# Kernel tuning notes

Measured on AMD Instinct MI355X. Metric: run time of the kernel, lower is better.

## Reference

```python
import jax, jax.numpy as jnp
import numpy as np

B, T, D, HS = 4, 2048, 1024, 64

def setup_inputs() -> dict:
    key = jax.random.key(0)
    kx, kk, kq, kv = jax.random.split(key, 4)
    scale = 1.0 / np.sqrt(D)
    return {
        "x": jax.random.normal(kx, (B, T, D), dtype=jnp.float32),
        "Wk": jax.random.normal(kk, (D, HS), dtype=jnp.float32) * scale,
        "Wq": jax.random.normal(kq, (D, HS), dtype=jnp.float32) * scale,
        "Wv": jax.random.normal(kv, (D, HS), dtype=jnp.float32) * scale,
    }

def reference(x, Wk, Wq, Wv):
    # x: [B, T, D]; projections to [B, T, HS]
    k = jnp.einsum("btd,dh->bth", x, Wk)
    q = jnp.einsum("btd,dh->bth", x, Wq)
    v = jnp.einsum("btd,dh->bth", x, Wv)
    # scores [B, T, T]; NOTE: original multiplies by sqrt(head_size) (faithful)
    att = jnp.einsum("bth,bsh->bts", q, k) * jnp.sqrt(jnp.float32(k.shape[-1]))
    Tq = x.shape[1]
    causal = jnp.tril(jnp.ones((Tq, Tq), dtype=bool))
    att = jnp.where(causal[None, :, :], att, -jnp.inf)
    p = jax.nn.softmax(att, axis=-1)
    # dropout = identity (eval mode)
    return jnp.einsum("bts,bsh->bth", p, v)
```

## Files before the change

kernel.cpp:

```cpp
#include <hip/hip_runtime.h>

#define Bn 4
#define Tn 2048
#define Dn 1024
#define HSn 64

typedef __attribute__((ext_vector_type(8))) short bf16x8;
typedef __attribute__((ext_vector_type(4))) float f32x4;
typedef __attribute__((ext_vector_type(4))) short s16x4;
typedef unsigned short u16;
typedef unsigned int u32;

__device__ __forceinline__ u16 f2bf_rne(float x) {
    u32 u = __float_as_uint(x);
    return (u16)((u + 0x7FFFu + ((u >> 16) & 1u)) >> 16);
}
__device__ __forceinline__ u16 f2bf_trunc(float x) {
    return (u16)(__float_as_uint(x) >> 16);
}
__device__ __forceinline__ float bf2f(u16 h) {
    return __uint_as_float(((u32)h) << 16);
}

#define GLL16(g, l)                                                        \
    __builtin_amdgcn_global_load_lds(                                      \
        (const __attribute__((address_space(1))) void*)(g),                \
        (__attribute__((address_space(3))) void*)(l), 16, 0, 0)

__global__ __launch_bounds__(256) void wprep_kernel(
    const float* __restrict__ Wk, const float* __restrict__ Wq,
    const float* __restrict__ Wv, u16* __restrict__ wtp)
{
    __shared__ float ws_[64][65];
    const int kb = blockIdx.x;
    const int w  = blockIdx.y;
    const float* __restrict__ W = (w == 0) ? Wk : (w == 1) ? Wq : Wv;
    const float scale = (w == 1) ? 8.0f : 1.0f;
    const int t = threadIdx.x;

    {
        const int kl = t >> 2, hq = t & 3;
        #pragma unroll
        for (int i = 0; i < 4; ++i) {
            float4 f = *(const float4*)(W + (size_t)(kb * 64 + kl) * 64 + hq * 16 + i * 4);
            ws_[kl][hq * 16 + i * 4 + 0] = f.x; ws_[kl][hq * 16 + i * 4 + 1] = f.y;
            ws_[kl][hq * 16 + i * 4 + 2] = f.z; ws_[kl][hq * 16 + i * 4 + 3] = f.w;
        }
    }
    __syncthreads();

    const int h = t & 63, quarter = t >> 6;
    const int n = w * 64 + h;
    const int ks = kb * 2 + (quarter >> 1);
    const int k_in0 = (quarter & 1) * 16;
    u16 hib[16], lob[16];
    #pragma unroll
    for (int j = 0; j < 16; ++j) {
        float v = ws_[quarter * 16 + j][h] * scale;
        u16 hi = f2bf_trunc(v);
        hib[j] = hi;
        lob[j] = f2bf_trunc(v - bf2f(hi));
    }
    u16* dst = wtp + (size_t)n * 2048 + ks * 64;
    *(uint4*)(dst + k_in0)          = *(const uint4*)&hib[0];
    *(uint4*)(dst + k_in0 + 8)      = *(const uint4*)&hib[8];
    *(uint4*)(dst + 32 + k_in0)     = *(const uint4*)&lob[0];
    *(uint4*)(dst + 32 + k_in0 + 8) = *(const uint4*)&lob[8];
}

#define NKS 32
#define XB(P) (smem + (P) * 4096)
#define BB(P) (smem + 12288 + (P) * 24576)

__global__ __launch_bounds__(512) void proj_gemm(
    const float* __restrict__ x, const u16* __restrict__ wtp,
    u16* __restrict__ qh8, u16* __restrict__ ql8,
    u16* __restrict__ kth, u16* __restrict__ ktl,
    u16* __restrict__ vtt)
{
    __shared__ __align__(16) unsigned char smem[86016];

    const int tid  = threadIdx.x;
    const int wave = tid >> 6, lane = tid & 63;
    const int lo4  = lane & 15, g = lane >> 4;
    const int row0 = blockIdx.x * 32;
    const int rt   = wave >> 2;
    const int cbase = (wave & 3) * 3;
    const int rl = rt * 16 + lo4;

    f32x4 acc[3];
    #pragma unroll
    for (int c = 0; c < 3; ++c) acc[c] = (f32x4){0.f, 0.f, 0.f, 0.f};

    const int xr = (tid >> 3) & 31, xc = tid & 7;
    const int xsw = (xc ^ (xr & 7)) << 2;
    const float* xsrc0 = x + (size_t)(row0 + xr) * Dn + xsw;

    #define STAGE(P, KS)                                                     \
        {                                                                    \
            if (tid < 256) GLL16(xsrc0 + (KS) * 32, XB(P) + tid * 16);       \
            _Pragma("unroll")                                                \
            for (int i = 0; i < 3; ++i) {                                    \
                const int c = i * 512 + tid;                                 \
                const int n_ = c >> 3, p_ = c & 7;                           \
                const int l_ = p_ ^ (n_ & 7);                                \
                const u16* src = wtp + (size_t)n_ * 2048 + (KS) * 64         \
                                 + ((l_ & 3) << 3) + ((l_ >> 2) << 5);       \
                GLL16(src, BB(P) + c * 16);                                  \
            }                                                                \
        }

    #define COMPUTE(P, KS)                                                   \
        {                                                                    \
            bf16x8 ah, al;                                                   \
            {                                                                \
                const unsigned char* xb = XB(P) + rl * 128;                  \
                f32x4 f0 = *(const f32x4*)(xb + (((2 * g + 0) ^ (rl & 7)) << 4)); \
                f32x4 f1 = *(const f32x4*)(xb + (((2 * g + 1) ^ (rl & 7)) << 4)); \
                _Pragma("unroll")                                            \
                for (int jj = 0; jj < 4; ++jj) {                             \
                    u16 h0 = f2bf_trunc(f0[jj]);                             \
                    ah[jj] = (short)h0;                                      \
                    al[jj] = (short)f2bf_trunc(f0[jj] - bf2f(h0));           \
                    u16 h1 = f2bf_trunc(f1[jj]);                             \
                    ah[4 + jj] = (short)h1;                                  \
                    al[4 + jj] = (short)f2bf_trunc(f1[jj] - bf2f(h1));       \
                }                                                            \
            }                                                                \
            _Pragma("unroll")                                                \
            for (int ct = 0; ct < 3; ++ct) {                                 \
                const int n = (cbase + ct) * 16 + lo4;                       \
                const unsigned char* bb = BB(P) + n * 128;                   \
                bf16x8 bh = *(const bf16x8*)(bb + (((g)     ^ (n & 7)) << 4)); \
                bf16x8 bl = *(const bf16x8*)(bb + (((4 + g) ^ (n & 7)) << 4)); \
                acc[ct] = __builtin_amdgcn_mfma_f32_16x16x32_bf16(ah, bh, acc[ct], 0, 0, 0); \
                acc[ct] = __builtin_amdgcn_mfma_f32_16x16x32_bf16(al, bh, acc[ct], 0, 0, 0); \
                acc[ct] = __builtin_amdgcn_mfma_f32_16x16x32_bf16(ah, bl, acc[ct], 0, 0, 0); \
            }                                                                \
        }

    STAGE(0, 0)
    STAGE(1, 1)
    int pb = 0;
    for (int ks = 0; ks < NKS; ++ks) {
        if (ks == NKS - 1) {
            asm volatile("s_waitcnt vmcnt(0)" ::: "memory");
        } else if (wave < 4) {
            asm volatile("s_waitcnt vmcnt(4)" ::: "memory");
        } else {
            asm volatile("s_waitcnt vmcnt(3)" ::: "memory");
        }
        __builtin_amdgcn_s_barrier();
        asm volatile("" ::: "memory");

        int ps = pb + 2; if (ps >= 3) ps -= 3;
        if (ks + 2 < NKS) STAGE(ps, ks + 2)
        COMPUTE(pb, ks)
        pb = (pb == 2) ? 0 : pb + 1;
    }

    const int grow = row0 + rt * 16 + g * 4;
    const int bb_ = grow >> 11, tl = grow & 2047;
    #pragma unroll
    for (int ct = 0; ct < 3; ++ct) {
        const int n = (cbase + ct) * 16 + lo4;
        if (n < 64) {
            const int ch = n >> 5, gi = (n >> 3) & 3, e = n & 7;
            const size_t base = (size_t)bb_ * 131072
                + (size_t)(((((tl >> 4) * 2 + ch) * 4 + gi) * 16 + (tl & 15)) * 8 + e);
            #pragma unroll
            for (int reg = 0; reg < 4; ++reg) {
                float v = acc[ct][reg];
                u16 hi = f2bf_trunc(v);
                kth[base + reg * 8] = hi;
                ktl[base + reg * 8] = f2bf_trunc(v - bf2f(hi));
            }
        } else if (n < 128) {
            #pragma unroll
            for (int reg = 0; reg < 4; ++reg) {
                float v = acc[ct][reg];
                u16 hi = f2bf_trunc(v);
                qh8[(size_t)(grow + reg) * HSn + (n - 64)] = hi;
                ql8[(size_t)(grow + reg) * HSn + (n - 64)] = f2bf_trunc(v - bf2f(hi));
            }
        } else {
            const int h = n - 128;
            s16x4 pack;
            #pragma unroll
            for (int reg = 0; reg < 4; ++reg)
                pack[reg] = (short)f2bf_rne(acc[ct][reg]);
            const size_t vidx = (size_t)bb_ * 131072
                + (size_t)((tl >> 5) * 2048 + (h >> 4) * 512 + (h & 15) * 32
                           + ((tl >> 3) & 3) * 8 + (tl & 7));
            *(s16x4*)(vtt + vidx) = pack;
        }
    }
}

struct KVset {
    bf16x8 kh0[2], kh1[2], kl0[2], kl1[2], vf[4];
};

__global__ __launch_bounds__(256, 2) void attn_kernel(
    const u16* __restrict__ qh8, const u16* __restrict__ ql8,
    const u16* __restrict__ kth, const u16* __restrict__ ktl,
    const u16* __restrict__ vtt, float* __restrict__ out)
{
    __shared__ __align__(16) unsigned char pbuf[4096];
    __shared__ __align__(16) float om_s[4][16][64];
    __shared__ float ml_s[4][16][2];

    const int tid  = threadIdx.x;
    const int wave = tid >> 6, lane = tid & 63;
    const int lo4  = lane & 15, g = lane >> 4;

    const int sblk = blockIdx.x >> 8, c = blockIdx.x & 255;
    const int tb = sblk ? 127 - (c >> 1) : (c >> 1);
    const int b  = 2 * sblk + (c & 1);
    const int t0 = tb * 16;

    const u16* qhp = qh8 + ((size_t)b * Tn + t0) * HSn;
    const u16* qlp = ql8 + ((size_t)b * Tn + t0) * HSn;
    const u16* kthb = kth + (size_t)b * 131072;
    const u16* ktlb = ktl + (size_t)b * 131072;
    const u16* vttb = vtt + (size_t)b * 131072;
    const int klane = lane * 8;
    const int vlane = lo4 * 32 + g * 8;

    bf16x8 qfh[2], qfl[2];
    #pragma unroll
    for (int ch = 0; ch < 2; ++ch) {
        qfh[ch] = *(const bf16x8*)(qhp + lo4 * HSn + ch * 32 + g * 8);
        qfl[ch] = *(const bf16x8*)(qlp + lo4 * HSn + ch * 32 + g * 8);
    }

    f32x4 O[4];
    #pragma unroll
    for (int n = 0; n < 4; ++n) O[n] = (f32x4){0.f, 0.f, 0.f, 0.f};
    float mrow[4], lrow[4];
    #pragma unroll
    for (int r = 0; r < 4; ++r) { mrow[r] = -1e30f; lrow[r] = 0.f; }

    const int nt = (t0 + 15) / 32 + 1;
    unsigned char* myPB = pbuf + wave * 1024;

    #define LOADSET(S, J)                                                     \
        {                                                                     \
            const u16* kb_ = kthb + (size_t)(2 * (J)) * 1024 + klane;         \
            const u16* lb_ = ktlb + (size_t)(2 * (J)) * 1024 + klane;         \
            S.kh0[0] = *(const bf16x8*)(kb_);                                 \
            S.kh1[0] = *(const bf16x8*)(kb_ + 512);                           \
            S.kh0[1] = *(const bf16x8*)(kb_ + 1024);                          \
            S.kh1[1] = *(const bf16x8*)(kb_ + 1536);                          \
            S.kl0[0] = *(const bf16x8*)(lb_);                                 \
            S.kl1[0] = *(const bf16x8*)(lb_ + 512);                           \
            S.kl0[1] = *(const bf16x8*)(lb_ + 1024);                          \
            S.kl1[1] = *(const bf16x8*)(lb_ + 1536);                          \
            const u16* vb_ = vttb + (size_t)(J) * 2048 + vlane;               \
            S.vf[0] = *(const bf16x8*)(vb_);                                  \
            S.vf[1] = *(const bf16x8*)(vb_ + 512);                            \
            S.vf[2] = *(const bf16x8*)(vb_ + 1024);                           \
            S.vf[3] = *(const bf16x8*)(vb_ + 1536);                           \
        }

    #define COMPUTE_ATT(S, J)                                                 \
        {                                                                     \
            const int s0 = (J) * 32;                                          \
            f32x4 accS[2];                                                    \
            __builtin_amdgcn_s_setprio(1);                                    \
            _Pragma("unroll")                                                 \
            for (int sb = 0; sb < 2; ++sb) {                                  \
                f32x4 a = (f32x4){0.f, 0.f, 0.f, 0.f};                        \
                a = __builtin_amdgcn_mfma_f32_16x16x32_bf16(qfh[0], S.kh0[sb], a, 0, 0, 0); \
                a = __builtin_amdgcn_mfma_f32_16x16x32_bf16(qfh[1], S.kh1[sb], a, 0, 0, 0); \
                a = __builtin_amdgcn_mfma_f32_16x16x32_bf16(qfl[0], S.kh0[sb], a, 0, 0, 0); \
                a = __builtin_amdgcn_mfma_f32_16x16x32_bf16(qfl[1], S.kh1[sb], a, 0, 0, 0); \
                a = __builtin_amdgcn_mfma_f32_16x16x32_bf16(qfh[0], S.kl0[sb], a, 0, 0, 0); \
                a = __builtin_amdgcn_mfma_f32_16x16x32_bf16(qfh[1], S.kl1[sb], a, 0, 0, 0); \
                accS[sb] = a;                                                 \
            }                                                                 \
            __builtin_amdgcn_s_setprio(0);                                    \
            _Pragma("unroll")                                                 \
            for (int reg = 0; reg < 4; ++reg) {                               \
                const int tg  = t0 + g * 4 + reg;                             \
                const int sg0 = s0 + lo4;                                     \
                const int sg1 = s0 + 16 + lo4;                                \
                float v0 = (sg0 <= tg) ? accS[0][reg] : -1e30f;               \
                float v1 = (sg1 <= tg) ? accS[1][reg] : -1e30f;               \
                float mt = fmaxf(v0, v1);                                     \
                mt = fmaxf(mt, __shfl_xor(mt, 1));                            \
                mt = fmaxf(mt, __shfl_xor(mt, 2));                            \
                mt = fmaxf(mt, __shfl_xor(mt, 4));                            \
                mt = fmaxf(mt, __shfl_xor(mt, 8));                            \
                float mn = fmaxf(mrow[reg], mt);                              \
                float p0 = (sg0 <= tg) ? __expf(v0 - mn) : 0.f;               \
                float p1 = (sg1 <= tg) ? __expf(v1 - mn) : 0.f;               \
                float ps = p0 + p1;                                           \
                ps += __shfl_xor(ps, 1);                                      \
                ps += __shfl_xor(ps, 2);                                      \
                ps += __shfl_xor(ps, 4);                                      \
                ps += __shfl_xor(ps, 8);                                      \
                float alpha = __expf(mrow[reg] - mn);                         \
                lrow[reg] = lrow[reg] * alpha + ps;                           \
                mrow[reg] = mn;                                               \
                _Pragma("unroll")                                             \
                for (int n = 0; n < 4; ++n) O[n][reg] *= alpha;               \
                const int irow = g * 4 + reg;                                 \
                *(u16*)(myPB + ((irow * 64 + lo4 * 2) ^ (reg << 4)))      = f2bf_rne(p0); \
                *(u16*)(myPB + ((irow * 64 + 32 + lo4 * 2) ^ (reg << 4))) = f2bf_rne(p1); \
            }                                                                 \
            bf16x8 pf = *(const bf16x8*)(myPB + ((lo4 * 64 + 16 * g) ^ ((lo4 & 3) << 4))); \
            __builtin_amdgcn_s_setprio(1);                                    \
            _Pragma("unroll")                                                 \
            for (int n = 0; n < 4; ++n)                                       \
                O[n] = __builtin_amdgcn_mfma_f32_16x16x32_bf16(pf, S.vf[n], O[n], 0, 0, 0); \
            __builtin_amdgcn_s_setprio(0);                                    \
        }

    KVset A, B;
    int j = wave;
    if (j < nt) LOADSET(A, j)
    while (j < nt) {
        if (j + 4 < nt) LOADSET(B, j + 4)
        COMPUTE_ATT(A, j)
        if (j + 4 < nt) {
            if (j + 8 < nt) LOADSET(A, j + 8)
            COMPUTE_ATT(B, j + 4)
        }
        j += 8;
    }

    #pragma unroll
    for (int n = 0; n < 4; ++n)
        #pragma unroll
        for (int reg = 0; reg < 4; ++reg)
            om_s[wave][g * 4 + reg][n * 16 + lo4] = O[n][reg];
    if (lo4 == 0) {
        #pragma unroll
        for (int reg = 0; reg < 4; ++reg) {
            ml_s[wave][g * 4 + reg][0] = mrow[reg];
            ml_s[wave][g * 4 + reg][1] = lrow[reg];
        }
    }
    __syncthreads();

    const int r  = tid >> 4;
    const int h4 = (tid & 15) * 4;
    float mw[4], lw[4], mstar = -1e30f;
    #pragma unroll
    for (int w = 0; w < 4; ++w) {
        mw[w] = ml_s[w][r][0];
        lw[w] = ml_s[w][r][1];
        mstar = fmaxf(mstar, mw[w]);
    }
    float lstar = 0.f, ew[4];
    #pragma unroll
    for (int w = 0; w < 4; ++w) { ew[w] = __expf(mw[w] - mstar); lstar += lw[w] * ew[w]; }
    float4 a4 = {0.f, 0.f, 0.f, 0.f};
    #pragma unroll
    for (int w = 0; w < 4; ++w) {
        float4 t4 = *(const float4*)&om_s[w][r][h4];
        a4.x += t4.x * ew[w]; a4.y += t4.y * ew[w];
        a4.z += t4.z * ew[w]; a4.w += t4.w * ew[w];
    }
    const float inv = 1.f / lstar;
    a4.x *= inv; a4.y *= inv; a4.z *= inv; a4.w *= inv;
    *(float4*)(out + ((size_t)b * Tn + t0 + r) * HSn + h4) = a4;
}

extern "C" void kernel_launch(void* const* d_in, const int* in_sizes, int n_in,
                              void* d_out, int out_size, void* d_ws, size_t ws_size,
                              hipStream_t stream) {
    const float* x  = (const float*)d_in[0];
    const float* Wk = (const float*)d_in[1];
    const float* Wq = (const float*)d_in[2];
    const float* Wv = (const float*)d_in[3];
    float* out = (float*)d_out;

    const size_t per = (size_t)Bn * Tn * HSn;
    u16* qh8 = (u16*)d_ws;
    u16* ql8 = qh8 + per;
    u16* kth = ql8 + per;
    u16* ktl = kth + per;
    u16* vtt = ktl + per;
    u16* wtp = vtt + per;

    hipLaunchKernelGGL(wprep_kernel, dim3(16, 3), dim3(256), 0, stream,
                       Wk, Wq, Wv, wtp);
    hipLaunchKernelGGL(proj_gemm, dim3(256), dim3(512), 0, stream,
                       x, wtp, qh8, ql8, kth, ktl, vtt);
    hipLaunchKernelGGL(attn_kernel, dim3(512), dim3(256), 0, stream,
                       qh8, ql8, kth, ktl, vtt, out);
}
```

Baseline: 49.48 us.

## Pre-swizzle weights into MFMA fragment layout and convert x once per tile

```diff
diff --git a/kernel.cpp b/kernel.cpp
--- a/kernel.cpp
+++ b/kernel.cpp
@@ -29,7 +29,7 @@
 
 __global__ __launch_bounds__(256) void wprep_kernel(
     const float* __restrict__ Wk, const float* __restrict__ Wq,
-    const float* __restrict__ Wv, u16* __restrict__ wtp)
+    const float* __restrict__ Wv, u16* __restrict__ wtp2)
 {
     __shared__ float ws_[64][65];
     const int kb = blockIdx.x;
@@ -50,9 +50,8 @@
     __syncthreads();
 
     const int h = t & 63, quarter = t >> 6;
-    const int n = w * 64 + h;
-    const int ks = kb * 2 + (quarter >> 1);
-    const int k_in0 = (quarter & 1) * 16;
+    const int nt = w * 4 + (h >> 4);
+    const int ksub = quarter >> 1;
     u16 hib[16], lob[16];
     #pragma unroll
     for (int j = 0; j < 16; ++j) {
@@ -61,24 +60,27 @@
         hib[j] = hi;
         lob[j] = f2bf_trunc(v - bf2f(hi));
     }
-    u16* dst = wtp + (size_t)n * 2048 + ks * 64;
-    *(uint4*)(dst + k_in0)          = *(const uint4*)&hib[0];
-    *(uint4*)(dst + k_in0 + 8)      = *(const uint4*)&hib[8];
-    *(uint4*)(dst + 32 + k_in0)     = *(const uint4*)&lob[0];
-    *(uint4*)(dst + 32 + k_in0 + 8) = *(const uint4*)&lob[8];
-}
-
-#define NKS 32
-#define XB(P) (smem + (P) * 4096)
-#define BB(P) (smem + 12288 + (P) * 24576)
+    const int lane0 = ((quarter * 2 + 0) & 3) * 16 + (h & 15);
+    const int lane1 = ((quarter * 2 + 1) & 3) * 16 + (h & 15);
+    u16* base = wtp2 + (size_t)kb * 24576 + (size_t)(ksub * 12 + nt) * 2 * 512;
+    *(uint4*)(base + lane0 * 8)       = *(const uint4*)&hib[0];
+    *(uint4*)(base + lane1 * 8)       = *(const uint4*)&hib[8];
+    *(uint4*)(base + 512 + lane0 * 8) = *(const uint4*)&lob[0];
+    *(uint4*)(base + 512 + lane1 * 8) = *(const uint4*)&lob[8];
+}
+
+#define NKB 16
+#define XHS(P) (smem + (P) * 4096)
+#define XLS(P) (smem + 8192 + (P) * 4096)
+#define BLSO(P) (smem + 16384 + (P) * 49152)
 
 __global__ __launch_bounds__(512) void proj_gemm(
-    const float* __restrict__ x, const u16* __restrict__ wtp,
+    const float* __restrict__ x, const u16* __restrict__ wtp2,
     u16* __restrict__ qh8, u16* __restrict__ ql8,
     u16* __restrict__ kth, u16* __restrict__ ktl,
     u16* __restrict__ vtt)
 {
-    __shared__ __align__(16) unsigned char smem[86016];
+    __shared__ __align__(16) unsigned char smem[114688];
 
     const int tid  = threadIdx.x;
     const int wave = tid >> 6, lane = tid & 63;
@@ -92,71 +94,83 @@
     #pragma unroll
     for (int c = 0; c < 3; ++c) acc[c] = (f32x4){0.f, 0.f, 0.f, 0.f};
 
-    const int xr = (tid >> 3) & 31, xc = tid & 7;
-    const int xsw = (xc ^ (xr & 7)) << 2;
-    const float* xsrc0 = x + (size_t)(row0 + xr) * Dn + xsw;
-
-    #define STAGE(P, KS)                                                     \
+    const int xr = tid >> 4, xc4 = (tid & 15) * 4;
+    const float* xsrc = x + (size_t)(row0 + xr) * Dn + xc4;
+    const int xwb = xr * 128 + (((xc4 >> 3) ^ (xr & 7)) << 4) + ((xc4 & 7) << 1);
+
+    #define STB(P, KB)                                                       \
         {                                                                    \
-            if (tid < 256) GLL16(xsrc0 + (KS) * 32, XB(P) + tid * 16);       \
             _Pragma("unroll")                                                \
-            for (int i = 0; i < 3; ++i) {                                    \
-                const int c = i * 512 + tid;                                 \
-                const int n_ = c >> 3, p_ = c & 7;                           \
-                const int l_ = p_ ^ (n_ & 7);                                \
-                const u16* src = wtp + (size_t)n_ * 2048 + (KS) * 64         \
-                                 + ((l_ & 3) << 3) + ((l_ >> 2) << 5);       \
-                GLL16(src, BB(P) + c * 16);                                  \
+            for (int i_ = 0; i_ < 6; ++i_) {                                 \
+                const int c_ = i_ * 512 + tid;                               \
+                GLL16(wtp2 + (size_t)(KB) * 24576 + c_ * 8, BLSO(P) + c_ * 16); \
             }                                                                \
         }
 
-    #define COMPUTE(P, KS)                                                   \
+    #define CONVW(P, XR)                                                     \
         {                                                                    \
-            bf16x8 ah, al;                                                   \
-            {                                                                \
-                const unsigned char* xb = XB(P) + rl * 128;                  \
-                f32x4 f0 = *(const f32x4*)(xb + (((2 * g + 0) ^ (rl & 7)) << 4)); \
-                f32x4 f1 = *(const f32x4*)(xb + (((2 * g + 1) ^ (rl & 7)) << 4)); \
+            u16 h0 = f2bf_trunc(XR[0]), h1 = f2bf_trunc(XR[1]);              \
+            u16 h2 = f2bf_trunc(XR[2]), h3 = f2bf_trunc(XR[3]);              \
+            u16 l0 = f2bf_trunc(XR[0] - bf2f(h0));                           \
+            u16 l1 = f2bf_trunc(XR[1] - bf2f(h1));                           \
+            u16 l2 = f2bf_trunc(XR[2] - bf2f(h2));                           \
+            u16 l3 = f2bf_trunc(XR[3] - bf2f(h3));                           \
+            uint2 hp, lp;                                                    \
+            hp.x = (u32)h0 | ((u32)h1 << 16); hp.y = (u32)h2 | ((u32)h3 << 16); \
+            lp.x = (u32)l0 | ((u32)l1 << 16); lp.y = (u32)l2 | ((u32)l3 << 16); \
+            *(uint2*)(XHS(P) + xwb) = hp;                                    \
+            *(uint2*)(XLS(P) + xwb) = lp;                                    \
+        }
+
+    #define PCOMP(P)                                                         \
+        {                                                                    \
+            _Pragma("unroll")                                                \
+            for (int ks_ = 0; ks_ < 2; ++ks_) {                              \
+                const int ch_ = ks_ * 4 + g;                                 \
+                const int aoff = rl * 128 + ((ch_ ^ (rl & 7)) << 4);         \
+                bf16x8 ah = *(const bf16x8*)(XHS(P) + aoff);                 \
+                bf16x8 al = *(const bf16x8*)(XLS(P) + aoff);                 \
                 _Pragma("unroll")                                            \
-                for (int jj = 0; jj < 4; ++jj) {                             \
-                    u16 h0 = f2bf_trunc(f0[jj]);                             \
-                    ah[jj] = (short)h0;                                      \
-                    al[jj] = (short)f2bf_trunc(f0[jj] - bf2f(h0));           \
-                    u16 h1 = f2bf_trunc(f1[jj]);                             \
-                    ah[4 + jj] = (short)h1;                                  \
-                    al[4 + jj] = (short)f2bf_trunc(f1[jj] - bf2f(h1));       \
+                for (int ct = 0; ct < 3; ++ct) {                             \
+                    const int ix = (ks_ * 12 + cbase + ct) * 2;              \
+                    bf16x8 bh = *(const bf16x8*)(BLSO(P) + ix * 1024 + lane * 16); \
+                    bf16x8 bl = *(const bf16x8*)(BLSO(P) + ix * 1024 + 1024 + lane * 16); \
+                    acc[ct] = __builtin_amdgcn_mfma_f32_16x16x32_bf16(ah, bh, acc[ct], 0, 0, 0); \
+                    acc[ct] = __builtin_amdgcn_mfma_f32_16x16x32_bf16(al, bh, acc[ct], 0, 0, 0); \
+                    acc[ct] = __builtin_amdgcn_mfma_f32_16x16x32_bf16(ah, bl, acc[ct], 0, 0, 0); \
                 }                                                            \
             }                                                                \
-            _Pragma("unroll")                                                \
-            for (int ct = 0; ct < 3; ++ct) {                                 \
-                const int n = (cbase + ct) * 16 + lo4;                       \
-                const unsigned char* bb = BB(P) + n * 128;                   \
-                bf16x8 bh = *(const bf16x8*)(bb + (((g)     ^ (n & 7)) << 4)); \
-                bf16x8 bl = *(const bf16x8*)(bb + (((4 + g) ^ (n & 7)) << 4)); \
-                acc[ct] = __builtin_amdgcn_mfma_f32_16x16x32_bf16(ah, bh, acc[ct], 0, 0, 0); \
-                acc[ct] = __builtin_amdgcn_mfma_f32_16x16x32_bf16(al, bh, acc[ct], 0, 0, 0); \
-                acc[ct] = __builtin_amdgcn_mfma_f32_16x16x32_bf16(ah, bl, acc[ct], 0, 0, 0); \
-            }                                                                \
-        }
-
-    STAGE(0, 0)
-    STAGE(1, 1)
-    int pb = 0;
-    for (int ks = 0; ks < NKS; ++ks) {
-        if (ks == NKS - 1) {
+        }
+
+    f32x4 xra = *(const f32x4*)(xsrc);
+    STB(0, 0)
+    f32x4 xrb = *(const f32x4*)(xsrc + 64);
+    CONVW(0, xra)
+    asm volatile("s_waitcnt vmcnt(1)" ::: "memory");
+    asm volatile("s_waitcnt lgkmcnt(0)" ::: "memory");
+    __builtin_amdgcn_s_barrier();
+
+    #pragma unroll
+    for (int kb = 0; kb < NKB; ++kb) {
+        if (kb + 1 < NKB) STB((kb + 1) & 1, kb + 1)
+        asm volatile("" ::: "memory");
+        if ((kb & 1) == 0) {
+            if (kb + 2 < NKB) xra = *(const f32x4*)(xsrc + (kb + 2) * 64);
+            if (kb + 1 < NKB) CONVW((kb + 1) & 1, xrb)
+        } else {
+            if (kb + 2 < NKB) xrb = *(const f32x4*)(xsrc + (kb + 2) * 64);
+            if (kb + 1 < NKB) CONVW((kb + 1) & 1, xra)
+        }
+        PCOMP(kb & 1)
+        if (kb + 2 < NKB) {
+            asm volatile("s_waitcnt vmcnt(1)" ::: "memory");
+        } else if (kb + 1 < NKB) {
             asm volatile("s_waitcnt vmcnt(0)" ::: "memory");
-        } else if (wave < 4) {
-            asm volatile("s_waitcnt vmcnt(4)" ::: "memory");
-        } else {
-            asm volatile("s_waitcnt vmcnt(3)" ::: "memory");
-        }
-        __builtin_amdgcn_s_barrier();
-        asm volatile("" ::: "memory");
-
-        int ps = pb + 2; if (ps >= 3) ps -= 3;
-        if (ks + 2 < NKS) STAGE(ps, ks + 2)
-        COMPUTE(pb, ks)
-        pb = (pb == 2) ? 0 : pb + 1;
+        }
+        if (kb + 1 < NKB) {
+            asm volatile("s_waitcnt lgkmcnt(0)" ::: "memory");
+            __builtin_amdgcn_s_barrier();
+        }
     }
 
     const int grow = row0 + rt * 16 + g * 4;
@@ -383,12 +397,12 @@
     u16* kth = ql8 + per;
     u16* ktl = kth + per;
     u16* vtt = ktl + per;
-    u16* wtp = vtt + per;
+    u16* wtp2 = vtt + per;
 
     hipLaunchKernelGGL(wprep_kernel, dim3(16, 3), dim3(256), 0, stream,
-                       Wk, Wq, Wv, wtp);
+                       Wk, Wq, Wv, wtp2);
     hipLaunchKernelGGL(proj_gemm, dim3(256), dim3(512), 0, stream,
-                       x, wtp, qh8, ql8, kth, ktl, vtt);
+                       x, wtp2, qh8, ql8, kth, ktl, vtt);
     hipLaunchKernelGGL(attn_kernel, dim3(512), dim3(256), 0, stream,
                        qh8, ql8, kth, ktl, vtt, out);
 }
```

Result: slower. 55.01 us (+11.2%).
